# Kernel optimization log

Hardware: AMD Instinct MI355X
Metric: run time of the kernel (lower is better)

## Reference

```python
import jax, jax.numpy as jnp
import numpy as np

B, T, C, H = 2, 2048, 1024, 16
HD = C // H
MAX_WAVELENGTH = 10000.0


def apply_rope(x, positions):
    # x: [B, H, T, HD], positions: [T]
    fraction = 2.0 * jnp.arange(HD // 2, dtype=jnp.float32) / HD
    timescale = MAX_WAVELENGTH ** fraction  # [HD//2]
    sinusoid = positions[:, None] / timescale[None, :]  # [T, HD//2]
    sin = jnp.sin(sinusoid)
    cos = jnp.cos(sinusoid)
    first, second = jnp.split(x, 2, axis=-1)
    out = jnp.concatenate(
        [first * cos - second * sin, second * cos + first * sin], axis=-1
    )
    return out.astype(x.dtype)


def setup_inputs() -> dict:
    key = jax.random.key(0)
    k1, k2, k3 = jax.random.split(key, 3)
    x = jax.random.normal(k1, (B, T, C), dtype=jnp.float32)
    w_attn = jax.random.normal(k2, (C, 3 * C), dtype=jnp.float32) * 0.02
    b_attn = jnp.zeros((3 * C,), dtype=jnp.float32)
    w_proj = jax.random.normal(k3, (C, C), dtype=jnp.float32) * 0.02
    b_proj = jnp.zeros((C,), dtype=jnp.float32)
    return {"x": x, "w_attn": w_attn, "b_attn": b_attn,
            "w_proj": w_proj, "b_proj": b_proj}


def reference(x, w_attn, b_attn, w_proj, b_proj):
    b, t, c = x.shape
    qkv = x @ w_attn + b_attn  # [B, T, 3C]
    q, k, v = jnp.split(qkv, 3, axis=-1)
    q = q.reshape(b, t, H, HD).transpose(0, 2, 1, 3)  # [B, H, T, HD]
    k = k.reshape(b, t, H, HD).transpose(0, 2, 1, 3)
    v = v.reshape(b, t, H, HD).transpose(0, 2, 1, 3)
    positions = jnp.arange(t, dtype=x.dtype)
    q = apply_rope(q, positions)
    k = apply_rope(k, positions)
    att = jnp.einsum('bhqd,bhkd->bhqk', q, k) * (1.0 / jnp.sqrt(HD))
    causal = jnp.tril(jnp.ones((t, t), dtype=bool))
    att = jnp.where(causal, att, jnp.finfo(att.dtype).min)
    att = jax.nn.softmax(att, axis=-1)
    y = jnp.einsum('bhqk,bhkd->bhqd', att, v)
    y = y.transpose(0, 2, 1, 3).reshape(b, t, c)
    return y @ w_proj + b_proj
```

## Files before the change

### kernel.cpp

```cpp
#include <hip/hip_runtime.h>
#include <hip/hip_bf16.h>


typedef __attribute__((ext_vector_type(8))) short short8;
typedef __attribute__((ext_vector_type(4))) float floatx4;

__device__ __forceinline__ unsigned short f2bf(float f) {
    union { float f; unsigned int u; } v; v.f = f;
    unsigned int r = v.u + 0x7FFFu + ((v.u >> 16) & 1u);
    return (unsigned short)(r >> 16);
}

__device__ __forceinline__ unsigned int pk2bf(float a, float b) {
    union { float f; unsigned int u; } ua, ub;
    ua.f = a; ub.f = b;
    return __builtin_amdgcn_perm(ub.u + 0x8000u, ua.u + 0x8000u, 0x07060302u);
}

__device__ __forceinline__ unsigned int cvtpk(float a, float b) {
    unsigned int r;
    asm("v_cvt_pk_bf16_f32 %0, %1, %2" : "=v"(r) : "v"(a), "v"(b));
    return r;
}

__device__ __forceinline__ void gld16(const void* g, void* l) {
    __builtin_amdgcn_global_load_lds(
        (const __attribute__((address_space(1))) unsigned int*)g,
        (__attribute__((address_space(3))) unsigned int*)l, 16, 0, 0);
}

__device__ __forceinline__ void transpose_body(
    const float* __restrict__ in, unsigned short* __restrict__ out,
    int R, int NC, int bx, int by, int tid,
    unsigned short (*tile)[68]) {
    int r0 = by * 64, c0 = bx * 64;
    int c4 = (tid & 15) * 4, rr = tid >> 4;
#pragma unroll
    for (int i = 0; i < 4; i++) {
        int row = rr + i * 16;
        float4 v = *(const float4*)&in[(size_t)(r0 + row) * NC + c0 + c4];
        ushort4 o;
        o.x = f2bf(v.x); o.y = f2bf(v.y); o.z = f2bf(v.z); o.w = f2bf(v.w);
        *(ushort4*)&tile[row][c4] = o;
    }
    __syncthreads();
    int col = tid & 63, rr2 = tid >> 6;
#pragma unroll
    for (int i = 0; i < 16; i++) {
        int orow = rr2 + i * 4;
        out[(size_t)(c0 + orow) * R + r0 + col] = tile[col][orow];
    }
}

__global__ __launch_bounds__(256) void prep(
    const float* __restrict__ x,
    const float* __restrict__ w_attn,
    const float* __restrict__ w_proj,
    unsigned short* __restrict__ x_bf,
    unsigned short* __restrict__ wTa,
    unsigned short* __restrict__ wTp,
    float2* __restrict__ tab) {
    __shared__ unsigned short tile[64][68];
    int bid = blockIdx.x;
    int tid = threadIdx.x;
    if (bid < 4096) {
        int i = bid * 256 + tid;
        float4 v = ((const float4*)x)[i];
        ushort4 o;
        o.x = f2bf(v.x); o.y = f2bf(v.y); o.z = f2bf(v.z); o.w = f2bf(v.w);
        ((ushort4*)x_bf)[i] = o;
    } else if (bid < 4864) {
        int t = bid - 4096;
        transpose_body(w_attn, wTa, 1024, 3072, t % 48, t / 48, tid, tile);
    } else if (bid < 5120) {
        int t = bid - 4864;
        transpose_body(w_proj, wTp, 1024, 1024, t & 15, t >> 4, tid, tile);
    } else {
        int i = (bid - 5120) * 256 + tid;
        int t = i >> 5, d = i & 31;
        float inv_ts = exp2f(-0.41524101186092036f * (float)d);
        float ang = (float)t * inv_ts;
        tab[i] = make_float2(sinf(ang), cosf(ang));
    }
}

__global__ __launch_bounds__(256) void gemm_qkv(
    const unsigned short* __restrict__ A,
    const unsigned short* __restrict__ BT,
    const float* __restrict__ bias,
    const float2* __restrict__ tab,
    unsigned short* __restrict__ qT,
    unsigned short* __restrict__ kT,
    unsigned short* __restrict__ vT) {
    __shared__ __align__(16) unsigned short smem[32768];
    int tid = threadIdx.x;
    int lane = tid & 63;
    int w = tid >> 6;
    int wx = w & 1, wy = w >> 1;
    int l16 = lane & 15, quad = lane >> 4;
    int lin = blockIdx.x;
    int xcd = lin & 7, idx = lin >> 3;
    int mb = (xcd >> 1) * 8 + idx / 12;
    int nb = (xcd & 1) * 12 + idx % 12;
    int m0 = mb * 128;
    int n0 = nb * 128;
    int x = l16 & 7;
    int lr = lane >> 3;
    int gc = (lane & 7) ^ lr;

    floatx4 acc[4][4];
#pragma unroll
    for (int mi = 0; mi < 4; mi++)
#pragma unroll
        for (int ni = 0; ni < 4; ni++)
            acc[mi][ni] = (floatx4){0.f, 0.f, 0.f, 0.f};

    auto stage = [&](int bsel, int k0) {
        unsigned short* as = smem + bsel * 16384;
        unsigned short* bs = as + 8192;
#pragma unroll
        for (int i = 0; i < 4; i++) {
            int seg = w * 4 + i;
            int row = seg * 8 + lr;
            gld16(A + (size_t)(m0 + row) * 1024 + k0 + gc * 8, &as[seg * 512]);
            gld16(BT + (size_t)(n0 + row) * 1024 + k0 + gc * 8, &bs[seg * 512]);
        }
    };

    auto compute = [&](int bsel) {
        const unsigned short* as = smem + bsel * 16384;
        const unsigned short* bs = as + 8192;
#pragma unroll
        for (int kk = 0; kk < 2; kk++) {
            short8 af[4], bf[4];
#pragma unroll
            for (int mi = 0; mi < 4; mi++) {
                int r = wy * 64 + mi * 16 + l16;
                af[mi] = *(const short8*)&as[r * 64 + (((kk << 2) | quad) ^ x) * 8];
            }
#pragma unroll
            for (int ni = 0; ni < 4; ni++) {
                int r = wx * 64 + ni * 16 + l16;
                bf[ni] = *(const short8*)&bs[r * 64 + (((kk << 2) | quad) ^ x) * 8];
            }
#pragma unroll
            for (int mi = 0; mi < 4; mi++)
#pragma unroll
                for (int ni = 0; ni < 4; ni++)
                    acc[mi][ni] = __builtin_amdgcn_mfma_f32_16x16x32_bf16(
                        af[mi], bf[ni], acc[mi][ni], 0, 0, 0);
        }
    };

    stage(0, 0);
    int cur = 0;
    for (int k0 = 0; k0 < 960; k0 += 64) {
        stage(cur ^ 1, k0 + 64);
        asm volatile("s_waitcnt vmcnt(8)" ::: "memory");
        __builtin_amdgcn_s_barrier();
        compute(cur);
        asm volatile("s_waitcnt lgkmcnt(0)" ::: "memory");
        __builtin_amdgcn_s_barrier();
        cur ^= 1;
    }
    asm volatile("s_waitcnt vmcnt(0)" ::: "memory");
    __builtin_amdgcn_s_barrier();
    compute(cur);
    __syncthreads();

    int region = n0 >> 10;
    int b = m0 >> 11;
    float b0 = bias[n0 + wx * 64 + l16];
    float b1 = bias[n0 + wx * 64 + 16 + l16];
    float b2 = bias[n0 + wx * 64 + 32 + l16];
    float b3 = bias[n0 + wx * 64 + 48 + l16];

    if (region < 2) {
        unsigned short* qk = region ? kT : qT;
        float scale = region ? 1.0f : 0.18033688011112042f;
        unsigned short* lq = smem;
#pragma unroll
        for (int mi = 0; mi < 4; mi++)
#pragma unroll
            for (int r = 0; r < 4; r++) {
                int tl = wy * 64 + mi * 16 + quad * 4 + r;
                int t = (m0 & 2047) + tl;
                float2 sc0 = tab[t * 32 + l16];
                float2 sc1 = tab[t * 32 + 16 + l16];
                float v1 = acc[mi][0][r] + b0, v2 = acc[mi][2][r] + b2;
                float w1 = acc[mi][1][r] + b1, w2 = acc[mi][3][r] + b3;
                unsigned short* orow = lq + tl * 136 + wx * 64;
                orow[l16]      = f2bf((v1 * sc0.y - v2 * sc0.x) * scale);
                orow[l16 + 32] = f2bf((v2 * sc0.y + v1 * sc0.x) * scale);
                orow[l16 + 16] = f2bf((w1 * sc1.y - w2 * sc1.x) * scale);
                orow[l16 + 48] = f2bf((w2 * sc1.y + w1 * sc1.x) * scale);
            }
        __syncthreads();
        int c8 = tid & 7;
        int hl = (tid >> 3) & 1;
        int tl0 = tid >> 4;
        int h = ((n0 & 1023) >> 6) + hl;
        unsigned short* ob = qk + (size_t)(b * 16 + h) * 2048 * 64;
#pragma unroll
        for (int p = 0; p < 8; p++) {
            int tl = p * 16 + tl0;
            int t = (m0 & 2047) + tl;
            short8 val = *(const short8*)&lq[tl * 136 + hl * 64 + c8 * 8];
            *(short8*)&ob[(size_t)t * 64 + c8 * 8] = val;
        }
    } else {
#pragma unroll
        for (int mi = 0; mi < 4; mi++)
#pragma unroll
            for (int ni = 0; ni < 4; ni++) {
                int d_loc = wx * 64 + ni * 16 + l16;
                int t_base = wy * 64 + mi * 16 + quad * 4;
                float bv = (ni == 0) ? b0 : (ni == 1) ? b1 : (ni == 2) ? b2 : b3;
                uint2 pk;
                pk.x = pk2bf(acc[mi][ni][0] + bv, acc[mi][ni][1] + bv);
                pk.y = pk2bf(acc[mi][ni][2] + bv, acc[mi][ni][3] + bv);
                int e = d_loc * 128 + (t_base ^ ((d_loc & 15) << 3));
                *(uint2*)&smem[e] = pk;
            }
        __syncthreads();
        int d_r = tid >> 1, half = tid & 1;
        int cv = (n0 - 2048) + d_r;
        int hh = cv >> 6, dd = cv & 63;
        int fofs = (d_r & 15) << 3;
        size_t vbase = ((size_t)(b * 16 + hh) * 64 + dd) * 2048 + (m0 & 2047);
#pragma unroll
        for (int c = 0; c < 8; c++) {
            int tc = half * 64 + c * 8;
            short8 val = *(const short8*)&smem[d_r * 128 + (tc ^ fofs)];
            *(short8*)&vT[vbase + tc] = val;
        }
    }
}

__global__ __launch_bounds__(256) void gemm_proj(
    const unsigned short* __restrict__ A,
    const unsigned short* __restrict__ BT,
    const float* __restrict__ bias,
    float* __restrict__ out) {
    __shared__ __align__(16) unsigned short smem[24576];
    int lane = threadIdx.x & 63;
    int w = threadIdx.x >> 6;
    int wx = w & 1, wy = w >> 1;
    int l16 = lane & 15, quad = lane >> 4;
    int lin = blockIdx.x;
    int swz = (lin & 7) * 64 + (lin >> 3);
    int m0 = (swz >> 4) * 128;
    int n0 = (swz & 15) * 64;
    int x = l16 & 7;
    int lr = lane >> 3;
    int gc = (lane & 7) ^ lr;

    floatx4 acc[4][2];
#pragma unroll
    for (int mi = 0; mi < 4; mi++)
#pragma unroll
        for (int ni = 0; ni < 2; ni++)
            acc[mi][ni] = (floatx4){0.f, 0.f, 0.f, 0.f};

    auto stage = [&](int bsel, int k0) {
        unsigned short* as = smem + bsel * 12288;
        unsigned short* bs = as + 8192;
#pragma unroll
        for (int i = 0; i < 6; i++) {
            int seg = w * 6 + i;
            if (seg < 16) {
                int row = seg * 8 + lr;
                gld16(A + (size_t)(m0 + row) * 1024 + k0 + gc * 8, &as[seg * 512]);
            } else {
                int s2 = seg - 16;
                int row = s2 * 8 + lr;
                gld16(BT + (size_t)(n0 + row) * 1024 + k0 + gc * 8, &bs[s2 * 512]);
            }
        }
    };

    auto compute = [&](int bsel) {
        const unsigned short* as = smem + bsel * 12288;
        const unsigned short* bs = as + 8192;
#pragma unroll
        for (int kk = 0; kk < 2; kk++) {
            short8 af[4], bf[2];
#pragma unroll
            for (int mi = 0; mi < 4; mi++) {
                int r = wy * 64 + mi * 16 + l16;
                af[mi] = *(const short8*)&as[r * 64 + (((kk << 2) | quad) ^ x) * 8];
            }
#pragma unroll
            for (int ni = 0; ni < 2; ni++) {
                int r = wx * 32 + ni * 16 + l16;
                bf[ni] = *(const short8*)&bs[r * 64 + (((kk << 2) | quad) ^ x) * 8];
            }
#pragma unroll
            for (int mi = 0; mi < 4; mi++)
#pragma unroll
                for (int ni = 0; ni < 2; ni++)
                    acc[mi][ni] = __builtin_amdgcn_mfma_f32_16x16x32_bf16(
                        af[mi], bf[ni], acc[mi][ni], 0, 0, 0);
        }
    };

    stage(0, 0);
    int cur = 0;
    for (int k0 = 0; k0 < 960; k0 += 64) {
        stage(cur ^ 1, k0 + 64);
        asm volatile("s_waitcnt vmcnt(6)" ::: "memory");
        __builtin_amdgcn_s_barrier();
        compute(cur);
        asm volatile("s_waitcnt lgkmcnt(0)" ::: "memory");
        __builtin_amdgcn_s_barrier();
        cur ^= 1;
    }
    asm volatile("s_waitcnt vmcnt(0)" ::: "memory");
    __builtin_amdgcn_s_barrier();
    compute(cur);

#pragma unroll
    for (int mi = 0; mi < 4; mi++)
#pragma unroll
        for (int ni = 0; ni < 2; ni++) {
            int row = m0 + wy * 64 + mi * 16 + quad * 4;
            int col = n0 + wx * 32 + ni * 16 + l16;
            float bv = bias[col];
#pragma unroll
            for (int r = 0; r < 4; r++)
                out[(size_t)(row + r) * 1024 + col] = acc[mi][ni][r] + bv;
        }
}

__global__ __launch_bounds__(256) void attn5(
    const unsigned short* __restrict__ qT,
    const unsigned short* __restrict__ kT,
    const unsigned short* __restrict__ vT,
    unsigned short* __restrict__ y) {
    __shared__ __align__(16) unsigned short kbuf[2][64 * 64];
    __shared__ __align__(16) unsigned short vbuf[2][64 * 64];
    __shared__ __align__(16) unsigned short pl[4][16 * 72];
    int lane = threadIdx.x & 63;
    int w = threadIdx.x >> 6;
    int l16 = lane & 15, quad = lane >> 4;
    int blk = blockIdx.x;
    int xcd = blk & 7, rix = blk >> 3;
    int bh = xcd * 4 + (rix & 3);
    int t = 31 - (rix >> 2);
    int b = bh >> 4, h = bh & 15;
    int q0 = t * 64 + w * 16;
    const unsigned short* qp = qT + (size_t)bh * 2048 * 64;
    unsigned short* plw = pl[w];
    int x = l16 & 7;

    short8 qf0 = *(const short8*)(qp + (size_t)(q0 + l16) * 64 + quad * 8);
    short8 qf1 = *(const short8*)(qp + (size_t)(q0 + l16) * 64 + 32 + quad * 8);

    short8 ones;
#pragma unroll
    for (int j = 0; j < 8; j++) ones[j] = (short)0x3F80;

    floatx4 acc[4];
#pragma unroll
    for (int ni = 0; ni < 4; ni++) acc[ni] = (floatx4){0.f, 0.f, 0.f, 0.f};
    floatx4 accl = (floatx4){0.f, 0.f, 0.f, 0.f};

    int lr8 = lane >> 3, l8 = lane & 7;
    const unsigned short* sp[4];
    unsigned short* ld0[4];
    int gstep;
    if (w < 2) {
        const unsigned short* kp = kT + (size_t)bh * 2048 * 64;
#pragma unroll
        for (int i = 0; i < 4; i++) {
            int seg = w * 4 + i;
            int row = seg * 8 + lr8;
            int c = l8 ^ (row & 7);
            sp[i] = kp + (size_t)row * 64 + c * 8;
            ld0[i] = &kbuf[0][seg * 512];
        }
        gstep = 4096;
    } else {
        const unsigned short* vp = vT + (size_t)bh * 64 * 2048;
#pragma unroll
        for (int i = 0; i < 4; i++) {
            int s = (w - 2) * 4 + i;
            int d = s * 8 + lr8;
            int c = l8 ^ (d & 7);
            sp[i] = vp + (size_t)d * 2048 + c * 8;
            ld0[i] = &vbuf[0][s * 512];
        }
        gstep = 64;
    }

    auto stage = [&](int bi) {
#pragma unroll
        for (int i = 0; i < 4; i++) {
            gld16(sp[i], ld0[i] + bi * 4096);
            sp[i] += gstep;
        }
    };

    int L = t + 1;
    int query = q0 + l16;
    stage(0);
    int cur = 0;
    for (int it = 0; it < L; it++) {
        if (it + 1 < L) {
            stage(cur ^ 1);
            asm volatile("s_waitcnt vmcnt(4)" ::: "memory");
        } else {
            asm volatile("s_waitcnt vmcnt(0)" ::: "memory");
        }
        __builtin_amdgcn_s_barrier();
        const unsigned short* kb = kbuf[cur];
        const unsigned short* vb = vbuf[cur];
        bool diag = (it == t);
        floatx4 s4[4];
        __builtin_amdgcn_s_setprio(1);
#pragma unroll
        for (int c = 0; c < 4; c++) {
            int r = c * 16 + l16;
            short8 kf0 = *(const short8*)&kb[r * 64 + ((quad) ^ x) * 8];
            short8 kf1 = *(const short8*)&kb[r * 64 + ((quad | 4) ^ x) * 8];
            floatx4 z = (floatx4){0.f, 0.f, 0.f, 0.f};
            z = __builtin_amdgcn_mfma_f32_16x16x32_bf16(kf0, qf0, z, 0, 0, 0);
            z = __builtin_amdgcn_mfma_f32_16x16x32_bf16(kf1, qf1, z, 0, 0, 0);
            s4[c] = z;
        }
        __builtin_amdgcn_s_setprio(0);
        int j0 = it * 64;
#pragma unroll
        for (int c = 0; c < 4; c++) {
            float p[4];
#pragma unroll
            for (int r = 0; r < 4; r++) {
                float e = __builtin_amdgcn_exp2f(s4[c][r]);
                if (diag) {
                    int key = j0 + c * 16 + quad * 4 + r;
                    e = (key <= query) ? e : 0.f;
                }
                p[r] = e;
            }
            uint2 pk;
            pk.x = cvtpk(p[0], p[1]);
            pk.y = cvtpk(p[2], p[3]);
            *(uint2*)&plw[l16 * 72 + c * 16 + quad * 4] = pk;
        }
        short8 pa0 = *(const short8*)&plw[l16 * 72 + quad * 8];
        short8 pa1 = *(const short8*)&plw[l16 * 72 + 32 + quad * 8];
        __builtin_amdgcn_s_setprio(1);
        accl = __builtin_amdgcn_mfma_f32_16x16x32_bf16(pa0, ones, accl, 0, 0, 0);
        accl = __builtin_amdgcn_mfma_f32_16x16x32_bf16(pa1, ones, accl, 0, 0, 0);
#pragma unroll
        for (int ni = 0; ni < 4; ni++) {
            int d = ni * 16 + l16;
            short8 vf0 = *(const short8*)&vb[d * 64 + ((quad) ^ x) * 8];
            short8 vf1 = *(const short8*)&vb[d * 64 + ((quad | 4) ^ x) * 8];
            acc[ni] = __builtin_amdgcn_mfma_f32_16x16x32_bf16(pa0, vf0, acc[ni], 0, 0, 0);
            acc[ni] = __builtin_amdgcn_mfma_f32_16x16x32_bf16(pa1, vf1, acc[ni], 0, 0, 0);
        }
        __builtin_amdgcn_s_setprio(0);
        asm volatile("s_waitcnt lgkmcnt(0)" ::: "memory");
        __builtin_amdgcn_s_barrier();
        cur ^= 1;
    }

    float inv[4];
#pragma unroll
    for (int r = 0; r < 4; r++) inv[r] = 1.f / accl[r];
#pragma unroll
    for (int ni = 0; ni < 4; ni++)
#pragma unroll
        for (int r = 0; r < 4; r++) {
            int tr = q0 + quad * 4 + r;
            y[((size_t)(b * 2048 + tr)) * 1024 + h * 64 + ni * 16 + l16] =
                f2bf(acc[ni][r] * inv[r]);
        }
}

extern "C" void kernel_launch(void* const* d_in, const int* in_sizes, int n_in,
                              void* d_out, int out_size, void* d_ws, size_t ws_size,
                              hipStream_t stream) {
    const float* x      = (const float*)d_in[0];
    const float* w_attn = (const float*)d_in[1];
    const float* b_attn = (const float*)d_in[2];
    const float* w_proj = (const float*)d_in[3];
    const float* b_proj = (const float*)d_in[4];
    float* out = (float*)d_out;

    char* ws = (char*)d_ws;
    unsigned short* x_bf = (unsigned short*)ws;
    unsigned short* wTa  = (unsigned short*)(ws + (8ull << 20));
    unsigned short* wTp  = (unsigned short*)(ws + (14ull << 20));
    unsigned short* qTb  = (unsigned short*)(ws + (16ull << 20));
    unsigned short* kTb  = (unsigned short*)(ws + (24ull << 20));
    unsigned short* vTb  = (unsigned short*)(ws + (32ull << 20));
    float2*         tab  = (float2*)(ws + (40ull << 20));
    unsigned short* y_bf = x_bf;

    prep<<<5376, 256, 0, stream>>>(x, w_attn, w_proj, x_bf, wTa, wTp, tab);
    gemm_qkv<<<768, 256, 0, stream>>>(x_bf, wTa, b_attn, tab, qTb, kTb, vTb);
    attn5<<<1024, 256, 0, stream>>>(qTb, kTb, vTb, y_bf);
    gemm_proj<<<512, 256, 0, stream>>>(y_bf, wTp, b_proj, out);
}
```

Before: 168.0 us.

## Use 8 waves per QKV GEMM block and restage RoPE epilogue through fp32 LDS

The QKV GEMM block grows to 512 threads in a 2x4 wave layout, so each wave owns a 64x32 sub-tile with half the accumulators. Because a wave no longer holds both RoPE halves of a head, the epilogue writes fp32 results to swizzled LDS and then applies the rotation per row. The attention kernel's block-to-(batch,head,tile) mapping also drops its XCD-aware grouping in favour of a plain mapping. The goal is more waves to hide latency and lower register pressure, at the cost of extra LDS traffic and barriers in the epilogue and a possible loss of L2 locality in attention.

```diff
diff --git a/kernel.cpp b/kernel.cpp
--- a/kernel.cpp
+++ b/kernel.cpp
@@ -84,7 +84,7 @@
     }
 }
 
-__global__ __launch_bounds__(256) void gemm_qkv(
+__global__ __launch_bounds__(512) void gemm_qkv(
     const unsigned short* __restrict__ A,
     const unsigned short* __restrict__ BT,
     const float* __restrict__ bias,
@@ -96,7 +96,7 @@
     int tid = threadIdx.x;
     int lane = tid & 63;
     int w = tid >> 6;
-    int wx = w & 1, wy = w >> 1;
+    int wx = w & 3, wy = w >> 2;
     int l16 = lane & 15, quad = lane >> 4;
     int lin = blockIdx.x;
     int xcd = lin & 7, idx = lin >> 3;
@@ -108,19 +108,19 @@
     int lr = lane >> 3;
     int gc = (lane & 7) ^ lr;
 
-    floatx4 acc[4][4];
+    floatx4 acc[4][2];
 #pragma unroll
     for (int mi = 0; mi < 4; mi++)
 #pragma unroll
-        for (int ni = 0; ni < 4; ni++)
+        for (int ni = 0; ni < 2; ni++)
             acc[mi][ni] = (floatx4){0.f, 0.f, 0.f, 0.f};
 
     auto stage = [&](int bsel, int k0) {
         unsigned short* as = smem + bsel * 16384;
         unsigned short* bs = as + 8192;
 #pragma unroll
-        for (int i = 0; i < 4; i++) {
-            int seg = w * 4 + i;
+        for (int i = 0; i < 2; i++) {
+            int seg = w * 2 + i;
             int row = seg * 8 + lr;
             gld16(A + (size_t)(m0 + row) * 1024 + k0 + gc * 8, &as[seg * 512]);
             gld16(BT + (size_t)(n0 + row) * 1024 + k0 + gc * 8, &bs[seg * 512]);
@@ -132,21 +132,21 @@
         const unsigned short* bs = as + 8192;
 #pragma unroll
         for (int kk = 0; kk < 2; kk++) {
-            short8 af[4], bf[4];
+            short8 af[4], bf[2];
 #pragma unroll
             for (int mi = 0; mi < 4; mi++) {
                 int r = wy * 64 + mi * 16 + l16;
                 af[mi] = *(const short8*)&as[r * 64 + (((kk << 2) | quad) ^ x) * 8];
             }
 #pragma unroll
-            for (int ni = 0; ni < 4; ni++) {
-                int r = wx * 64 + ni * 16 + l16;
+            for (int ni = 0; ni < 2; ni++) {
+                int r = wx * 32 + ni * 16 + l16;
                 bf[ni] = *(const short8*)&bs[r * 64 + (((kk << 2) | quad) ^ x) * 8];
             }
 #pragma unroll
             for (int mi = 0; mi < 4; mi++)
 #pragma unroll
-                for (int ni = 0; ni < 4; ni++)
+                for (int ni = 0; ni < 2; ni++)
                     acc[mi][ni] = __builtin_amdgcn_mfma_f32_16x16x32_bf16(
                         af[mi], bf[ni], acc[mi][ni], 0, 0, 0);
         }
@@ -156,7 +156,7 @@
     int cur = 0;
     for (int k0 = 0; k0 < 960; k0 += 64) {
         stage(cur ^ 1, k0 + 64);
-        asm volatile("s_waitcnt vmcnt(8)" ::: "memory");
+        asm volatile("s_waitcnt vmcnt(4)" ::: "memory");
         __builtin_amdgcn_s_barrier();
         compute(cur);
         asm volatile("s_waitcnt lgkmcnt(0)" ::: "memory");
@@ -170,52 +170,75 @@
 
     int region = n0 >> 10;
     int b = m0 >> 11;
-    float b0 = bias[n0 + wx * 64 + l16];
-    float b1 = bias[n0 + wx * 64 + 16 + l16];
-    float b2 = bias[n0 + wx * 64 + 32 + l16];
-    float b3 = bias[n0 + wx * 64 + 48 + l16];
+    float b0 = bias[n0 + wx * 32 + l16];
+    float b1 = bias[n0 + wx * 32 + 16 + l16];
 
     if (region < 2) {
         unsigned short* qk = region ? kT : qT;
         float scale = region ? 1.0f : 0.18033688011112042f;
+        float* F = (float*)smem;
+#pragma unroll
+        for (int mi = 0; mi < 4; mi++)
+#pragma unroll
+            for (int ni = 0; ni < 2; ni++) {
+                float bv = ni ? b1 : b0;
+                int col = wx * 32 + ni * 16 + l16;
+#pragma unroll
+                for (int r = 0; r < 4; r++) {
+                    int row = wy * 64 + mi * 16 + quad * 4 + r;
+                    F[row * 128 + (col ^ ((row & 7) << 2))] = acc[mi][ni][r] + bv;
+                }
+            }
+        __syncthreads();
+        int tl = tid >> 2, qq = tid & 3;
+        int hl = qq >> 1, d0 = (qq & 1) * 16;
+        int t = (m0 & 2047) + tl;
+        int xr = (tl & 7) << 2;
+        unsigned int lo[8], hi[8];
+#pragma unroll
+        for (int j = 0; j < 8; j++) {
+            float o1[2], o2[2];
+#pragma unroll
+            for (int e = 0; e < 2; e++) {
+                int d = d0 + j * 2 + e;
+                float v1 = F[tl * 128 + ((hl * 64 + d) ^ xr)];
+                float v2 = F[tl * 128 + ((hl * 64 + d + 32) ^ xr)];
+                float2 sc = tab[t * 32 + d];
+                o1[e] = (v1 * sc.y - v2 * sc.x) * scale;
+                o2[e] = (v2 * sc.y + v1 * sc.x) * scale;
+            }
+            lo[j] = (unsigned int)f2bf(o1[0]) | ((unsigned int)f2bf(o1[1]) << 16);
+            hi[j] = (unsigned int)f2bf(o2[0]) | ((unsigned int)f2bf(o2[1]) << 16);
+        }
+        __syncthreads();
         unsigned short* lq = smem;
-#pragma unroll
-        for (int mi = 0; mi < 4; mi++)
-#pragma unroll
-            for (int r = 0; r < 4; r++) {
-                int tl = wy * 64 + mi * 16 + quad * 4 + r;
-                int t = (m0 & 2047) + tl;
-                float2 sc0 = tab[t * 32 + l16];
-                float2 sc1 = tab[t * 32 + 16 + l16];
-                float v1 = acc[mi][0][r] + b0, v2 = acc[mi][2][r] + b2;
-                float w1 = acc[mi][1][r] + b1, w2 = acc[mi][3][r] + b3;
-                unsigned short* orow = lq + tl * 136 + wx * 64;
-                orow[l16]      = f2bf((v1 * sc0.y - v2 * sc0.x) * scale);
-                orow[l16 + 32] = f2bf((v2 * sc0.y + v1 * sc0.x) * scale);
-                orow[l16 + 16] = f2bf((w1 * sc1.y - w2 * sc1.x) * scale);
-                orow[l16 + 48] = f2bf((w2 * sc1.y + w1 * sc1.x) * scale);
-            }
+        int base = tl * 136 + hl * 64 + d0;
+#pragma unroll
+        for (int j = 0; j < 4; j++) {
+            *(uint2*)&lq[base + 4 * j] = make_uint2(lo[2 * j], lo[2 * j + 1]);
+            *(uint2*)&lq[base + 32 + 4 * j] = make_uint2(hi[2 * j], hi[2 * j + 1]);
+        }
         __syncthreads();
         int c8 = tid & 7;
-        int hl = (tid >> 3) & 1;
+        int hl2 = (tid >> 3) & 1;
         int tl0 = tid >> 4;
-        int h = ((n0 & 1023) >> 6) + hl;
+        int h = ((n0 & 1023) >> 6) + hl2;
         unsigned short* ob = qk + (size_t)(b * 16 + h) * 2048 * 64;
 #pragma unroll
-        for (int p = 0; p < 8; p++) {
-            int tl = p * 16 + tl0;
-            int t = (m0 & 2047) + tl;
-            short8 val = *(const short8*)&lq[tl * 136 + hl * 64 + c8 * 8];
-            *(short8*)&ob[(size_t)t * 64 + c8 * 8] = val;
+        for (int p = 0; p < 4; p++) {
+            int tl_ = p * 32 + tl0;
+            int tt = (m0 & 2047) + tl_;
+            short8 val = *(const short8*)&lq[tl_ * 136 + hl2 * 64 + c8 * 8];
+            *(short8*)&ob[(size_t)tt * 64 + c8 * 8] = val;
         }
     } else {
 #pragma unroll
         for (int mi = 0; mi < 4; mi++)
 #pragma unroll
-            for (int ni = 0; ni < 4; ni++) {
-                int d_loc = wx * 64 + ni * 16 + l16;
+            for (int ni = 0; ni < 2; ni++) {
+                int d_loc = wx * 32 + ni * 16 + l16;
                 int t_base = wy * 64 + mi * 16 + quad * 4;
-                float bv = (ni == 0) ? b0 : (ni == 1) ? b1 : (ni == 2) ? b2 : b3;
+                float bv = ni ? b1 : b0;
                 uint2 pk;
                 pk.x = pk2bf(acc[mi][ni][0] + bv, acc[mi][ni][1] + bv);
                 pk.y = pk2bf(acc[mi][ni][2] + bv, acc[mi][ni][3] + bv);
@@ -223,14 +246,14 @@
                 *(uint2*)&smem[e] = pk;
             }
         __syncthreads();
-        int d_r = tid >> 1, half = tid & 1;
+        int d_r = tid >> 2, qtr = tid & 3;
         int cv = (n0 - 2048) + d_r;
         int hh = cv >> 6, dd = cv & 63;
         int fofs = (d_r & 15) << 3;
         size_t vbase = ((size_t)(b * 16 + hh) * 64 + dd) * 2048 + (m0 & 2047);
 #pragma unroll
-        for (int c = 0; c < 8; c++) {
-            int tc = half * 64 + c * 8;
+        for (int c = 0; c < 4; c++) {
+            int tc = qtr * 32 + c * 8;
             short8 val = *(const short8*)&smem[d_r * 128 + (tc ^ fofs)];
             *(short8*)&vT[vbase + tc] = val;
         }
@@ -344,9 +367,8 @@
     int w = threadIdx.x >> 6;
     int l16 = lane & 15, quad = lane >> 4;
     int blk = blockIdx.x;
-    int xcd = blk & 7, rix = blk >> 3;
-    int bh = xcd * 4 + (rix & 3);
-    int t = 31 - (rix >> 2);
+    int t = 31 - (blk >> 5);
+    int bh = blk & 31;
     int b = bh >> 4, h = bh & 15;
     int q0 = t * 64 + w * 16;
     const unsigned short* qp = qT + (size_t)bh * 2048 * 64;
@@ -500,7 +522,7 @@
     unsigned short* y_bf = x_bf;
 
     prep<<<5376, 256, 0, stream>>>(x, w_attn, w_proj, x_bf, wTa, wTp, tab);
-    gemm_qkv<<<768, 256, 0, stream>>>(x_bf, wTa, b_attn, tab, qTb, kTb, vTb);
+    gemm_qkv<<<768, 512, 0, stream>>>(x_bf, wTa, b_attn, tab, qTb, kTb, vTb);
     attn5<<<1024, 256, 0, stream>>>(qTb, kTb, vTb, y_bf);
     gemm_proj<<<512, 256, 0, stream>>>(y_bf, wTp, b_proj, out);
 }
```

After: 162.1 us. 1.04x faster.
